# Optimization experiments

Measured on AMD Instinct MI355X. Metric: run time of the kernel, lower is better.

The kernel has to match this reference:

```python
import jax, jax.numpy as jnp
import numpy as np

B, S, H, I, NH, E = 16, 512, 1024, 4096, 16, 8
DH = H // NH
EPS = 1e-12


def layer_norm(x, g, b):
    mu = jnp.mean(x, axis=-1, keepdims=True)
    var = jnp.mean(jnp.square(x - mu), axis=-1, keepdims=True)
    return (x - mu) * jax.lax.rsqrt(var + EPS) * g + b


def setup_inputs() -> dict:
    key = jax.random.key(0)
    ks = jax.random.split(key, 16)
    s_h = 1.0 / np.sqrt(H)
    s_i = 1.0 / np.sqrt(I)
    return {
        "hidden_states": jax.random.normal(ks[0], (B, S, H), jnp.float32),
        "Wq": jax.random.normal(ks[1], (H, H), jnp.float32) * s_h,
        "bq": jnp.zeros((H,), jnp.float32),
        "Wk": jax.random.normal(ks[2], (H, H), jnp.float32) * s_h,
        "bk": jnp.zeros((H,), jnp.float32),
        "Wv": jax.random.normal(ks[3], (H, H), jnp.float32) * s_h,
        "bv": jnp.zeros((H,), jnp.float32),
        "Wo": jax.random.normal(ks[4], (H, H), jnp.float32) * s_h,
        "bo": jnp.zeros((H,), jnp.float32),
        "ln1_g": jnp.ones((H,), jnp.float32),
        "ln1_b": jnp.zeros((H,), jnp.float32),
        "ln2_g": jnp.ones((H,), jnp.float32),
        "ln2_b": jnp.zeros((H,), jnp.float32),
        "gate_W": jax.random.normal(ks[5], (H, E), jnp.float32) * s_h,
        "W_up": jax.random.normal(ks[6], (E, H, I), jnp.float32) * s_h,
        "b_up": jnp.zeros((E, I), jnp.float32),
        "W_down": jax.random.normal(ks[7], (E, I, H), jnp.float32) * s_i,
        "b_down": jnp.zeros((E, H), jnp.float32),
    }


def reference(hidden_states, Wq, bq, Wk, bk, Wv, bv, Wo, bo,
              ln1_g, ln1_b, ln2_g, ln2_b, gate_W, W_up, b_up, W_down, b_down):
    x = hidden_states
    # --- BERT self-attention ---
    q = (x @ Wq + bq).reshape(B, S, NH, DH)
    k = (x @ Wk + bk).reshape(B, S, NH, DH)
    v = (x @ Wv + bv).reshape(B, S, NH, DH)
    scores = jnp.einsum("bqhd,bkhd->bhqk", q, k) / np.sqrt(DH)
    probs = jax.nn.softmax(scores, axis=-1)
    ctx = jnp.einsum("bhqk,bkhd->bqhd", probs, v).reshape(B, S, H)
    # BertSelfOutput: dense + residual + LayerNorm
    attn_out = layer_norm(ctx @ Wo + bo + x, ln1_g, ln1_b)

    # --- feed_forward_chunk: pre-LN, MoE, residual (residual on attn_out) ---
    x_ln = layer_norm(attn_out, ln2_g, ln2_b)
    router_output = jnp.einsum("bsh,he->bse", x_ln, gate_W)
    router_logits = jnp.mean(router_output, axis=1)          # [B, E]
    choice = jnp.argmax(router_logits, axis=-1)              # softmax-argmax == logits-argmax

    # per-sample top-1 expert: gather each sample's expert weights, batched GEMM
    Wu = W_up[choice]                                        # [B, H, I]
    Wd = W_down[choice]                                      # [B, I, H]
    h = jax.nn.gelu(jnp.einsum("bsh,bhi->bsi", x_ln, Wu) + b_up[choice][:, None, :],
                    approximate=False)
    moe = jnp.einsum("bsi,bih->bsh", h, Wd) + b_down[choice][:, None, :]
    layer_output = moe + attn_out
    return (layer_output, router_logits)
```

## Files before the change

kernel.cpp:

```cpp
#include <hip/hip_runtime.h>


typedef __attribute__((ext_vector_type(4))) float f32x4;
typedef __attribute__((ext_vector_type(8))) short s8v;
typedef __attribute__((ext_vector_type(4))) short s4v;
typedef unsigned short u16;

#define DEV static __device__ __forceinline__

DEV u16 f2bf(float f){
  union { float f; unsigned u; } v; v.f = f;
  unsigned r = v.u + 0x7fffu + ((v.u >> 16) & 1u);
  return (u16)(r >> 16);
}

DEV f32x4 mfma16(s8v a, s8v b, f32x4 c){
  return __builtin_amdgcn_mfma_f32_16x16x32_bf16(a, b, c, 0, 0, 0);
}

DEV float wave_sum(float s){
#pragma unroll
  for (int o = 1; o < 64; o <<= 1) s += __shfl_xor(s, o);
  return s;
}

#define ASYNC_COPY16(g, l) \
  __builtin_amdgcn_global_load_lds((const __attribute__((address_space(1))) void*)(g), \
                                   (__attribute__((address_space(3))) void*)(l), 16, 0, 0)

__global__ __launch_bounds__(256) void cvt_bf16(const float* __restrict__ in,
                                                u16* __restrict__ out)
{
  const size_t i = ((size_t)blockIdx.x * 256 + threadIdx.x) * 8;
  f32x4 a = *(const f32x4*)&in[i];
  f32x4 b = *(const f32x4*)&in[i + 4];
  s8v o;
#pragma unroll
  for (int j = 0; j < 4; ++j){ o[j] = (short)f2bf(a[j]); o[4 + j] = (short)f2bf(b[j]); }
  *(s8v*)&out[i] = o;
}

__global__ __launch_bounds__(256) void transpose_w(const float* __restrict__ in,
                                                   u16* __restrict__ out, int R, int C)
{
  __shared__ float t[64][65];
  const size_t bs = (size_t)blockIdx.z * R * (size_t)C;
  in += bs; out += bs;
  const int c0 = blockIdx.x * 64, r0 = blockIdx.y * 64;
  const int tx = threadIdx.x & 63, ty = threadIdx.x >> 6;
#pragma unroll
  for (int j = 0; j < 64; j += 4) t[ty + j][tx] = in[(size_t)(r0 + ty + j) * C + c0 + tx];
  __syncthreads();
#pragma unroll
  for (int j = 0; j < 64; j += 4) out[(size_t)(c0 + ty + j) * R + r0 + tx] = f2bf(t[tx][ty + j]);
}

template<int MODE>
__global__ __launch_bounds__(256, 2) void gemm_bt(
    const u16* __restrict__ A, const u16* __restrict__ Bt,
    const float* __restrict__ bias, void* __restrict__ outp,
    const float* __restrict__ resid, int M, int N, int K,
    const int* __restrict__ choice,
    long aBatch, long outBatch, long residBatch, long btExpert, long biasExpert)
{
  const int z = blockIdx.z;
  if (choice){
    const int e = choice[z];
    Bt   += (size_t)e * btExpert;
    bias += (size_t)e * biasExpert;
  }
  A += (size_t)z * aBatch;

  const int tid = threadIdx.x;
  const int lane = tid & 63, wid = tid >> 6;
  const int hi = lane >> 4, l15 = lane & 15;
  const int wr = wid >> 1, wc = wid & 1;
  const long row0 = (long)blockIdx.x * 128;
  const long col0 = (long)blockIdx.y * 128;

  __shared__ __align__(16) u16 lA[128 * 32];
  __shared__ __align__(16) u16 lB[128 * 32];

  f32x4 acc[4][4];
#pragma unroll
  for (int i = 0; i < 4; ++i)
#pragma unroll
    for (int j = 0; j < 4; ++j) acc[i][j] = f32x4{0.f, 0.f, 0.f, 0.f};

  const int c1 = tid, c2 = tid + 256;
  const u16* sA1 = A  + (row0 + (c1 >> 2)) * (size_t)K + (c1 & 3) * 8;
  const u16* sA2 = A  + (row0 + (c2 >> 2)) * (size_t)K + (c2 & 3) * 8;
  const u16* sB1 = Bt + (col0 + (c1 >> 2)) * (size_t)K + (c1 & 3) * 8;
  const u16* sB2 = Bt + (col0 + (c2 >> 2)) * (size_t)K + (c2 & 3) * 8;
  u16* dA1 = &lA[c1 * 8]; u16* dA2 = &lA[c2 * 8];
  u16* dB1 = &lB[c1 * 8]; u16* dB2 = &lB[c2 * 8];

  for (int kt = 0; kt < K; kt += 32){
    ASYNC_COPY16(sA1, dA1);
    ASYNC_COPY16(sA2, dA2);
    ASYNC_COPY16(sB1, dB1);
    ASYNC_COPY16(sB2, dB2);
    sA1 += 32; sA2 += 32; sB1 += 32; sB2 += 32;
    asm volatile("s_waitcnt vmcnt(0)" ::: "memory");
    __syncthreads();

    s8v af[4], bf[4];
#pragma unroll
    for (int mi = 0; mi < 4; ++mi)
      af[mi] = *(const s8v*)&lA[(wr * 64 + mi * 16 + l15) * 32 + hi * 8];
#pragma unroll
    for (int ni = 0; ni < 4; ++ni)
      bf[ni] = *(const s8v*)&lB[(wc * 64 + ni * 16 + l15) * 32 + hi * 8];
#pragma unroll
    for (int mi = 0; mi < 4; ++mi)
#pragma unroll
      for (int ni = 0; ni < 4; ++ni)
        acc[mi][ni] = mfma16(af[mi], bf[ni], acc[mi][ni]);
    __syncthreads();
  }

#pragma unroll
  for (int mi = 0; mi < 4; ++mi){
    const long rowb = row0 + wr * 64 + mi * 16 + hi * 4;
#pragma unroll
    for (int ni = 0; ni < 4; ++ni){
      const long col = col0 + wc * 64 + ni * 16 + l15;
      const float bv = bias[col];
#pragma unroll
      for (int r = 0; r < 4; ++r){
        const long row = rowb + r;
        float v = acc[mi][ni][r] + bv;
        if (MODE == 2){
          float* o = (float*)outp + (size_t)z * outBatch;
          const float* rs = resid + (size_t)z * residBatch;
          o[row * N + col] = v + rs[row * N + col];
        } else if (MODE == 0){
          u16* o = (u16*)outp + (size_t)z * outBatch;
          o[row * N + col] = f2bf(v);
        } else if (MODE == 1){
          u16* o = (u16*)outp + (size_t)z * outBatch;
          const float gv = 0.5f * v * (1.0f + erff(v * 0.70710678118654752f));
          o[row * N + col] = f2bf(gv);
        } else {
          const int bb = (int)(row >> 9), ss = (int)(row & 511);
          const int hh = (int)(col >> 6), dd = (int)(col & 63);
          ((u16*)outp)[(((size_t)(bb * 16 + hh)) * 64 + dd) * 512 + ss] = f2bf(v);
        }
      }
    }
  }
}

__global__ __launch_bounds__(256) void attn_fwd(
    const u16* __restrict__ qb, const u16* __restrict__ kb,
    const u16* __restrict__ vt, u16* __restrict__ ctx)
{
  const int tid = threadIdx.x;
  const int lane = tid & 63, wid = tid >> 6;
  const int hi = lane >> 4, l15 = lane & 15;
  const int h = blockIdx.y, b = blockIdx.z;
  const int q0 = blockIdx.x * 128 + wid * 32;

  const u16* kp0 = kb + (size_t)b * 512 * 1024 + h * 64;
  const u16* vp0 = vt + ((size_t)(b * 16 + h)) * 64 * 512;

  __shared__ __align__(16) u16 lK[2][64 * 64];
  __shared__ __align__(16) u16 lV[2][64 * 64];
  __shared__ __align__(16) u16 lP[4][2][16][72];

#define STAGE(bsel, k0s) do { \
  _Pragma("unroll") \
  for (int i = 0; i < 2; ++i){ \
    const int idx = i * 256 + tid; \
    const int row = idx >> 3, seg = idx & 7; \
    const int sc = ((seg ^ (row & 7)) << 3); \
    ASYNC_COPY16(kp0 + (size_t)((k0s) + row) * 1024 + sc, &lK[bsel][idx * 8]); \
    ASYNC_COPY16(vp0 + (size_t)row * 512 + (k0s) + sc,    &lV[bsel][idx * 8]); \
  } \
} while (0)

  const u16* qp = qb + ((size_t)b * 512 + q0) * 1024 + h * 64;
  s8v qf[2][2];
#pragma unroll
  for (int qt = 0; qt < 2; ++qt)
#pragma unroll
    for (int st = 0; st < 2; ++st)
      qf[qt][st] = *(const s8v*)&qp[(size_t)(qt * 16 + l15) * 1024 + st * 32 + hi * 8];

  f32x4 o[2][4];
#pragma unroll
  for (int qt = 0; qt < 2; ++qt)
#pragma unroll
    for (int mi = 0; mi < 4; ++mi) o[qt][mi] = f32x4{0.f, 0.f, 0.f, 0.f};
  float mrun[2] = {-3e38f, -3e38f}, lrun[2] = {0.f, 0.f};

  STAGE(0, 0);
  __syncthreads();

  for (int t = 0; t < 8; ++t){
    const int buf = t & 1;
    if (t < 7) STAGE(buf ^ 1, (t + 1) * 64);

    f32x4 s[2][4];
#pragma unroll
    for (int qt = 0; qt < 2; ++qt)
#pragma unroll
      for (int kt = 0; kt < 4; ++kt) s[qt][kt] = f32x4{0.f, 0.f, 0.f, 0.f};
#pragma unroll
    for (int st = 0; st < 2; ++st){
      s8v kf[4];
#pragma unroll
      for (int kt = 0; kt < 4; ++kt){
        const int row = kt * 16 + l15;
        kf[kt] = *(const s8v*)&lK[buf][row * 64 + (((st * 4 + hi) ^ (row & 7)) << 3)];
      }
#pragma unroll
      for (int qt = 0; qt < 2; ++qt)
#pragma unroll
        for (int kt = 0; kt < 4; ++kt)
          s[qt][kt] = mfma16(kf[kt], qf[qt][st], s[qt][kt]);
    }

#pragma unroll
    for (int qt = 0; qt < 2; ++qt){
      float mx = s[qt][0][0];
#pragma unroll
      for (int kt = 0; kt < 4; ++kt)
#pragma unroll
        for (int r = 0; r < 4; ++r) mx = fmaxf(mx, s[qt][kt][r]);
      mx *= 0.125f;
      mx = fmaxf(mx, __shfl_xor(mx, 16));
      mx = fmaxf(mx, __shfl_xor(mx, 32));
      const float mnew = fmaxf(mrun[qt], mx);
      const float alpha = __expf(mrun[qt] - mnew);
      mrun[qt] = mnew;
      float ps = 0.f;
#pragma unroll
      for (int kt = 0; kt < 4; ++kt){
        s4v pk;
#pragma unroll
        for (int r = 0; r < 4; ++r){
          const float p = __expf(s[qt][kt][r] * 0.125f - mnew);
          ps += p; pk[r] = (short)f2bf(p);
        }
        *(s4v*)&lP[wid][qt][l15][kt * 16 + 4 * hi] = pk;
      }
      ps += __shfl_xor(ps, 16);
      ps += __shfl_xor(ps, 32);
      lrun[qt] = lrun[qt] * alpha + ps;
#pragma unroll
      for (int mi = 0; mi < 4; ++mi)
#pragma unroll
        for (int r = 0; r < 4; ++r) o[qt][mi][r] *= alpha;
    }

#pragma unroll
    for (int ks = 0; ks < 2; ++ks){
      s8v vf[4];
#pragma unroll
      for (int mi = 0; mi < 4; ++mi){
        const int row = mi * 16 + l15;
        vf[mi] = *(const s8v*)&lV[buf][row * 64 + (((ks * 4 + hi) ^ (row & 7)) << 3)];
      }
#pragma unroll
      for (int qt = 0; qt < 2; ++qt){
        const s8v pf = *(const s8v*)&lP[wid][qt][l15][ks * 32 + 8 * hi];
#pragma unroll
        for (int mi = 0; mi < 4; ++mi)
          o[qt][mi] = mfma16(vf[mi], pf, o[qt][mi]);
      }
    }
    __syncthreads();
  }
#undef STAGE

#pragma unroll
  for (int qt = 0; qt < 2; ++qt){
    const float inv = 1.f / lrun[qt];
    u16* cp = ctx + ((size_t)b * 512 + q0 + qt * 16 + l15) * 1024 + h * 64;
#pragma unroll
    for (int mi = 0; mi < 4; ++mi)
#pragma unroll
      for (int r = 0; r < 4; ++r)
        cp[mi * 16 + 4 * hi + r] = f2bf(o[qt][mi][r] * inv);
  }
}

__global__ __launch_bounds__(256, 2) void ln_inplace(float* __restrict__ x,
    const float* __restrict__ g, const float* __restrict__ be)
{
  const int row = blockIdx.x * 4 + (threadIdx.x >> 6);
  const int lane = threadIdx.x & 63;
  float* p = x + (size_t)row * 1024;
  f32x4 v[4];
#pragma unroll
  for (int c = 0; c < 4; ++c) v[c] = *(const f32x4*)&p[c * 256 + lane * 4];
  float s = 0.f;
#pragma unroll
  for (int c = 0; c < 4; ++c){ s += v[c][0] + v[c][1] + v[c][2] + v[c][3]; }
  const float mu = wave_sum(s) * (1.f / 1024.f);
  float s2 = 0.f;
#pragma unroll
  for (int c = 0; c < 4; ++c)
#pragma unroll
    for (int j = 0; j < 4; ++j){ const float d = v[c][j] - mu; s2 += d * d; }
  const float rs = rsqrtf(wave_sum(s2) * (1.f / 1024.f) + 1e-12f);
#pragma unroll
  for (int c = 0; c < 4; ++c){
    const f32x4 gg = *(const f32x4*)&g[c * 256 + lane * 4];
    const f32x4 bb = *(const f32x4*)&be[c * 256 + lane * 4];
    f32x4 ov;
#pragma unroll
    for (int j = 0; j < 4; ++j) ov[j] = (v[c][j] - mu) * rs * gg[j] + bb[j];
    *(f32x4*)&p[c * 256 + lane * 4] = ov;
  }
}

__global__ __launch_bounds__(256, 2) void ln2_colsum(
    const float* __restrict__ attn, const float* __restrict__ g, const float* __restrict__ be,
    u16* __restrict__ xln, float* __restrict__ colsum)
{
  const int b = blockIdx.y;
  const int wid = threadIdx.x >> 6, lane = threadIdx.x & 63;
  __shared__ float cacc[1024];
  for (int i = threadIdx.x; i < 1024; i += 256) cacc[i] = 0.f;
  __syncthreads();
  float acc[16];
#pragma unroll
  for (int i = 0; i < 16; ++i) acc[i] = 0.f;
  const int rbase = b * 512 + blockIdx.x * 64 + wid * 16;
  for (int rr = 0; rr < 16; ++rr){
    const float* p = attn + (size_t)(rbase + rr) * 1024;
    f32x4 v[4];
#pragma unroll
    for (int c = 0; c < 4; ++c) v[c] = *(const f32x4*)&p[c * 256 + lane * 4];
    float s = 0.f;
#pragma unroll
    for (int c = 0; c < 4; ++c) s += v[c][0] + v[c][1] + v[c][2] + v[c][3];
    const float mu = wave_sum(s) * (1.f / 1024.f);
    float s2 = 0.f;
#pragma unroll
    for (int c = 0; c < 4; ++c)
#pragma unroll
      for (int j = 0; j < 4; ++j){ const float d = v[c][j] - mu; s2 += d * d; }
    const float rs = rsqrtf(wave_sum(s2) * (1.f / 1024.f) + 1e-12f);
    u16* op = xln + (size_t)(rbase + rr) * 1024;
#pragma unroll
    for (int c = 0; c < 4; ++c){
      const f32x4 gg = *(const f32x4*)&g[c * 256 + lane * 4];
      const f32x4 bb = *(const f32x4*)&be[c * 256 + lane * 4];
      s4v ov;
#pragma unroll
      for (int j = 0; j < 4; ++j){
        const float y = (v[c][j] - mu) * rs * gg[j] + bb[j];
        acc[c * 4 + j] += y;
        ov[j] = (short)f2bf(y);
      }
      *(s4v*)&op[c * 256 + lane * 4] = ov;
    }
  }
#pragma unroll
  for (int c = 0; c < 4; ++c)
#pragma unroll
    for (int j = 0; j < 4; ++j)
      atomicAdd(&cacc[c * 256 + lane * 4 + j], acc[c * 4 + j]);
  __syncthreads();
  for (int i = threadIdx.x; i < 1024; i += 256) atomicAdd(&colsum[b * 1024 + i], cacc[i]);
}

__global__ void router_argmax(const float* __restrict__ colsum, const float* __restrict__ gate,
                              float* __restrict__ logits, int* __restrict__ choice)
{
  const int b = blockIdx.x, lane = threadIdx.x;
  float pa[8];
#pragma unroll
  for (int e = 0; e < 8; ++e) pa[e] = 0.f;
  for (int it = 0; it < 16; ++it){
    const int hh = it * 64 + lane;
    const float c = colsum[b * 1024 + hh];
    const float* gp = gate + (size_t)hh * 8;
#pragma unroll
    for (int e = 0; e < 8; ++e) pa[e] += c * gp[e];
  }
#pragma unroll
  for (int e = 0; e < 8; ++e) pa[e] = wave_sum(pa[e]);
  if (lane == 0){
    float best = -3e38f; int bi = 0;
#pragma unroll
    for (int e = 0; e < 8; ++e){
      const float lg = pa[e] * (1.f / 512.f);
      logits[b * 8 + e] = lg;
      if (lg > best){ best = lg; bi = e; }
    }
    choice[b] = bi;
  }
}

extern "C" void kernel_launch(void* const* d_in, const int* in_sizes, int n_in,
                              void* d_out, int out_size, void* d_ws, size_t ws_size,
                              hipStream_t stream)
{
  const float* x    = (const float*)d_in[0];
  const float* Wq   = (const float*)d_in[1];
  const float* bq   = (const float*)d_in[2];
  const float* Wk   = (const float*)d_in[3];
  const float* bk   = (const float*)d_in[4];
  const float* Wv   = (const float*)d_in[5];
  const float* bv   = (const float*)d_in[6];
  const float* Wo   = (const float*)d_in[7];
  const float* bo   = (const float*)d_in[8];
  const float* ln1g = (const float*)d_in[9];
  const float* ln1b = (const float*)d_in[10];
  const float* ln2g = (const float*)d_in[11];
  const float* ln2b = (const float*)d_in[12];
  const float* gate = (const float*)d_in[13];
  const float* Wup  = (const float*)d_in[14];
  const float* bup  = (const float*)d_in[15];
  const float* Wdn  = (const float*)d_in[16];
  const float* bdn  = (const float*)d_in[17];

  size_t off = 0;
  char* wsb = (char*)d_ws;
  auto take = [&](size_t n) -> void* {
    void* p = wsb + off; off += (n + 255) & ~(size_t)255; return p;
  };
  u16*   x_bf  = (u16*)take(8192ull * 1024 * 2);
  u16*   Wqt   = (u16*)take(1024ull * 1024 * 2);
  u16*   Wkt   = (u16*)take(1024ull * 1024 * 2);
  u16*   Wvt   = (u16*)take(1024ull * 1024 * 2);
  u16*   Wot   = (u16*)take(1024ull * 1024 * 2);
  u16*   q_bf  = (u16*)take(8192ull * 1024 * 2);
  u16*   k_bf  = (u16*)take(8192ull * 1024 * 2);
  u16*   vt_bf = (u16*)take(8192ull * 1024 * 2);
  float* tmp   = (float*)take(8192ull * 1024 * 4);
  u16*   Wupt  = (u16*)take(8ull * 4096 * 1024 * 2);
  u16*   Wdnt  = (u16*)take(8ull * 1024 * 4096 * 2);
  u16*   h_bf  = (u16*)take(8192ull * 4096 * 2);
  float* colsum = (float*)take(16ull * 1024 * 4);
  int*   choice = (int*)take(256);

  u16* ctx = x_bf;
  u16* xln = q_bf;
  float* logits = (float*)d_out + 8388608;

  cvt_bf16<<<4096, 256, 0, stream>>>(x, x_bf);
  transpose_w<<<dim3(16, 16, 1), 256, 0, stream>>>(Wq,  Wqt,  1024, 1024);
  transpose_w<<<dim3(16, 16, 1), 256, 0, stream>>>(Wk,  Wkt,  1024, 1024);
  transpose_w<<<dim3(16, 16, 1), 256, 0, stream>>>(Wv,  Wvt,  1024, 1024);
  transpose_w<<<dim3(16, 16, 1), 256, 0, stream>>>(Wo,  Wot,  1024, 1024);
  transpose_w<<<dim3(64, 16, 8), 256, 0, stream>>>(Wup, Wupt, 1024, 4096);
  transpose_w<<<dim3(16, 64, 8), 256, 0, stream>>>(Wdn, Wdnt, 4096, 1024);

  gemm_bt<0><<<dim3(64, 8, 1), 256, 0, stream>>>(x_bf, Wqt, bq, q_bf,  nullptr,
      8192, 1024, 1024, nullptr, 0, 0, 0, 0, 0);
  gemm_bt<0><<<dim3(64, 8, 1), 256, 0, stream>>>(x_bf, Wkt, bk, k_bf,  nullptr,
      8192, 1024, 1024, nullptr, 0, 0, 0, 0, 0);
  gemm_bt<3><<<dim3(64, 8, 1), 256, 0, stream>>>(x_bf, Wvt, bv, vt_bf, nullptr,
      8192, 1024, 1024, nullptr, 0, 0, 0, 0, 0);

  attn_fwd<<<dim3(4, 16, 16), 256, 0, stream>>>(q_bf, k_bf, vt_bf, ctx);

  gemm_bt<2><<<dim3(64, 8, 1), 256, 0, stream>>>(ctx, Wot, bo, tmp, x,
      8192, 1024, 1024, nullptr, 0, 0, 0, 0, 0);
  ln_inplace<<<2048, 256, 0, stream>>>(tmp, ln1g, ln1b);

  hipMemsetAsync(colsum, 0, 16 * 1024 * sizeof(float), stream);
  ln2_colsum<<<dim3(8, 16), 256, 0, stream>>>(tmp, ln2g, ln2b, xln, colsum);
  router_argmax<<<16, 64, 0, stream>>>(colsum, gate, logits, choice);

  gemm_bt<1><<<dim3(4, 32, 16), 256, 0, stream>>>(xln, Wupt, bup, h_bf, nullptr,
      512, 4096, 1024, choice, 512ll * 1024, 512ll * 4096, 0, 4096ll * 1024, 4096);
  gemm_bt<2><<<dim3(4, 8, 16), 256, 0, stream>>>(h_bf, Wdnt, bdn, d_out, tmp,
      512, 1024, 4096, choice, 512ll * 4096, 512ll * 1024, 512ll * 1024, 1024ll * 4096, 1024);
}
```

Measured before the change: 552.7 us.

## Fuse QKV GEMM, merge both LayerNorms, double-buffer GEMM LDS, swizzle MoE blocks

The three Q/K/V projections become one N=3072 GEMM, relying on the transposed weights sitting contiguously in the workspace and on a concatenated bias. A new epilogue mode routes each column segment to q, k or the transposed v layout. LN1 and LN2 are merged into one pass that writes attn_out and the bf16 LN2 output and accumulates the router column sums, which removes a separate full-tensor read and write. The GEMM mainloop now uses two LDS buffers so the next K tile's async copy is issued before the current tile's MFMAs, and the MoE GEMMs remap block IDs across XCDs for better L2 locality. The loads are no longer followed by an explicit vmcnt wait, so correctness depends on the barrier waiting for the async copies, and the larger LDS footprint may reduce occupancy.

```diff
diff --git a/kernel.cpp b/kernel.cpp
--- a/kernel.cpp
+++ b/kernel.cpp
@@ -55,15 +55,26 @@
   for (int j = 0; j < 64; j += 4) out[(size_t)(c0 + ty + j) * R + r0 + tx] = f2bf(t[tx][ty + j]);
 }
 
-template<int MODE>
+template<int MODE, bool SWZ>
 __global__ __launch_bounds__(256, 2) void gemm_bt(
     const u16* __restrict__ A, const u16* __restrict__ Bt,
     const float* __restrict__ bias, void* __restrict__ outp,
     const float* __restrict__ resid, int M, int N, int K,
     const int* __restrict__ choice,
-    long aBatch, long outBatch, long residBatch, long btExpert, long biasExpert)
-{
-  const int z = blockIdx.z;
+    long aBatch, long outBatch, long residBatch, long btExpert, long biasExpert,
+    void* __restrict__ out2, void* __restrict__ out3)
+{
+  int bx, by, bz;
+  if (SWZ){
+    const int nx = gridDim.x, ny = gridDim.y;
+    const int nwg = nx * ny * gridDim.z;
+    int id = blockIdx.x + nx * (blockIdx.y + ny * blockIdx.z);
+    if ((nwg & 7) == 0){ const int q = nwg >> 3; id = (id & 7) * q + (id >> 3); }
+    bx = id % nx; const int r2 = id / nx; by = r2 % ny; bz = r2 / ny;
+  } else {
+    bx = blockIdx.x; by = blockIdx.y; bz = blockIdx.z;
+  }
+  const int z = bz;
   if (choice){
     const int e = choice[z];
     Bt   += (size_t)e * btExpert;
@@ -75,11 +86,11 @@
   const int lane = tid & 63, wid = tid >> 6;
   const int hi = lane >> 4, l15 = lane & 15;
   const int wr = wid >> 1, wc = wid & 1;
-  const long row0 = (long)blockIdx.x * 128;
-  const long col0 = (long)blockIdx.y * 128;
-
-  __shared__ __align__(16) u16 lA[128 * 32];
-  __shared__ __align__(16) u16 lB[128 * 32];
+  const long row0 = (long)bx * 128;
+  const long col0 = (long)by * 128;
+
+  __shared__ __align__(16) u16 lA[2][128 * 32];
+  __shared__ __align__(16) u16 lB[2][128 * 32];
 
   f32x4 acc[4][4];
 #pragma unroll
@@ -92,32 +103,37 @@
   const u16* sA2 = A  + (row0 + (c2 >> 2)) * (size_t)K + (c2 & 3) * 8;
   const u16* sB1 = Bt + (col0 + (c1 >> 2)) * (size_t)K + (c1 & 3) * 8;
   const u16* sB2 = Bt + (col0 + (c2 >> 2)) * (size_t)K + (c2 & 3) * 8;
-  u16* dA1 = &lA[c1 * 8]; u16* dA2 = &lA[c2 * 8];
-  u16* dB1 = &lB[c1 * 8]; u16* dB2 = &lB[c2 * 8];
-
-  for (int kt = 0; kt < K; kt += 32){
-    ASYNC_COPY16(sA1, dA1);
-    ASYNC_COPY16(sA2, dA2);
-    ASYNC_COPY16(sB1, dB1);
-    ASYNC_COPY16(sB2, dB2);
-    sA1 += 32; sA2 += 32; sB1 += 32; sB2 += 32;
-    asm volatile("s_waitcnt vmcnt(0)" ::: "memory");
+
+#define GSTAGE(bsel) do { \
+  ASYNC_COPY16(sA1, &lA[bsel][c1 * 8]); \
+  ASYNC_COPY16(sA2, &lA[bsel][c2 * 8]); \
+  ASYNC_COPY16(sB1, &lB[bsel][c1 * 8]); \
+  ASYNC_COPY16(sB2, &lB[bsel][c2 * 8]); \
+  sA1 += 32; sA2 += 32; sB1 += 32; sB2 += 32; \
+} while (0)
+
+  const int nk = K >> 5;
+  GSTAGE(0);
+  __syncthreads();
+
+  for (int t = 0; t < nk; ++t){
+    const int cur = t & 1;
+    if (t + 1 < nk) GSTAGE(cur ^ 1);
+    s8v af[4], bfr[4];
+#pragma unroll
+    for (int mi = 0; mi < 4; ++mi)
+      af[mi] = *(const s8v*)&lA[cur][(wr * 64 + mi * 16 + l15) * 32 + hi * 8];
+#pragma unroll
+    for (int ni = 0; ni < 4; ++ni)
+      bfr[ni] = *(const s8v*)&lB[cur][(wc * 64 + ni * 16 + l15) * 32 + hi * 8];
+#pragma unroll
+    for (int mi = 0; mi < 4; ++mi)
+#pragma unroll
+      for (int ni = 0; ni < 4; ++ni)
+        acc[mi][ni] = mfma16(af[mi], bfr[ni], acc[mi][ni]);
     __syncthreads();
-
-    s8v af[4], bf[4];
-#pragma unroll
-    for (int mi = 0; mi < 4; ++mi)
-      af[mi] = *(const s8v*)&lA[(wr * 64 + mi * 16 + l15) * 32 + hi * 8];
-#pragma unroll
-    for (int ni = 0; ni < 4; ++ni)
-      bf[ni] = *(const s8v*)&lB[(wc * 64 + ni * 16 + l15) * 32 + hi * 8];
-#pragma unroll
-    for (int mi = 0; mi < 4; ++mi)
-#pragma unroll
-      for (int ni = 0; ni < 4; ++ni)
-        acc[mi][ni] = mfma16(af[mi], bf[ni], acc[mi][ni]);
-    __syncthreads();
-  }
+  }
+#undef GSTAGE
 
 #pragma unroll
   for (int mi = 0; mi < 4; ++mi){
@@ -141,10 +157,20 @@
           u16* o = (u16*)outp + (size_t)z * outBatch;
           const float gv = 0.5f * v * (1.0f + erff(v * 0.70710678118654752f));
           o[row * N + col] = f2bf(gv);
-        } else {
+        } else if (MODE == 3){
           const int bb = (int)(row >> 9), ss = (int)(row & 511);
           const int hh = (int)(col >> 6), dd = (int)(col & 63);
           ((u16*)outp)[(((size_t)(bb * 16 + hh)) * 64 + dd) * 512 + ss] = f2bf(v);
+        } else {
+          const int seg = (int)(col >> 10), lc = (int)(col & 1023);
+          const u16 bv16 = f2bf(v);
+          if (seg == 0)      ((u16*)outp)[row * 1024 + lc] = bv16;
+          else if (seg == 1) ((u16*)out2)[row * 1024 + lc] = bv16;
+          else {
+            const int bb = (int)(row >> 9), ss = (int)(row & 511);
+            const int hh = lc >> 6, dd = lc & 63;
+            ((u16*)out3)[(((size_t)(bb * 16 + hh)) * 64 + dd) * 512 + ss] = bv16;
+          }
         }
       }
     }
@@ -286,38 +312,9 @@
   }
 }
 
-__global__ __launch_bounds__(256, 2) void ln_inplace(float* __restrict__ x,
-    const float* __restrict__ g, const float* __restrict__ be)
-{
-  const int row = blockIdx.x * 4 + (threadIdx.x >> 6);
-  const int lane = threadIdx.x & 63;
-  float* p = x + (size_t)row * 1024;
-  f32x4 v[4];
-#pragma unroll
-  for (int c = 0; c < 4; ++c) v[c] = *(const f32x4*)&p[c * 256 + lane * 4];
-  float s = 0.f;
-#pragma unroll
-  for (int c = 0; c < 4; ++c){ s += v[c][0] + v[c][1] + v[c][2] + v[c][3]; }
-  const float mu = wave_sum(s) * (1.f / 1024.f);
-  float s2 = 0.f;
-#pragma unroll
-  for (int c = 0; c < 4; ++c)
-#pragma unroll
-    for (int j = 0; j < 4; ++j){ const float d = v[c][j] - mu; s2 += d * d; }
-  const float rs = rsqrtf(wave_sum(s2) * (1.f / 1024.f) + 1e-12f);
-#pragma unroll
-  for (int c = 0; c < 4; ++c){
-    const f32x4 gg = *(const f32x4*)&g[c * 256 + lane * 4];
-    const f32x4 bb = *(const f32x4*)&be[c * 256 + lane * 4];
-    f32x4 ov;
-#pragma unroll
-    for (int j = 0; j < 4; ++j) ov[j] = (v[c][j] - mu) * rs * gg[j] + bb[j];
-    *(f32x4*)&p[c * 256 + lane * 4] = ov;
-  }
-}
-
-__global__ __launch_bounds__(256, 2) void ln2_colsum(
-    const float* __restrict__ attn, const float* __restrict__ g, const float* __restrict__ be,
+__global__ __launch_bounds__(256, 2) void ln12_colsum(
+    float* __restrict__ t, const float* __restrict__ g1, const float* __restrict__ b1,
+    const float* __restrict__ g2, const float* __restrict__ b2,
     u16* __restrict__ xln, float* __restrict__ colsum)
 {
   const int b = blockIdx.y;
@@ -330,7 +327,7 @@
   for (int i = 0; i < 16; ++i) acc[i] = 0.f;
   const int rbase = b * 512 + blockIdx.x * 64 + wid * 16;
   for (int rr = 0; rr < 16; ++rr){
-    const float* p = attn + (size_t)(rbase + rr) * 1024;
+    float* p = t + (size_t)(rbase + rr) * 1024;
     f32x4 v[4];
 #pragma unroll
     for (int c = 0; c < 4; ++c) v[c] = *(const f32x4*)&p[c * 256 + lane * 4];
@@ -344,15 +341,34 @@
 #pragma unroll
       for (int j = 0; j < 4; ++j){ const float d = v[c][j] - mu; s2 += d * d; }
     const float rs = rsqrtf(wave_sum(s2) * (1.f / 1024.f) + 1e-12f);
+    float y1s = 0.f;
+#pragma unroll
+    for (int c = 0; c < 4; ++c){
+      const f32x4 gg = *(const f32x4*)&g1[c * 256 + lane * 4];
+      const f32x4 bb = *(const f32x4*)&b1[c * 256 + lane * 4];
+#pragma unroll
+      for (int j = 0; j < 4; ++j){
+        v[c][j] = (v[c][j] - mu) * rs * gg[j] + bb[j];
+        y1s += v[c][j];
+      }
+      *(f32x4*)&p[c * 256 + lane * 4] = v[c];
+    }
+    const float mu2 = wave_sum(y1s) * (1.f / 1024.f);
+    float s22 = 0.f;
+#pragma unroll
+    for (int c = 0; c < 4; ++c)
+#pragma unroll
+      for (int j = 0; j < 4; ++j){ const float d = v[c][j] - mu2; s22 += d * d; }
+    const float rs2 = rsqrtf(wave_sum(s22) * (1.f / 1024.f) + 1e-12f);
     u16* op = xln + (size_t)(rbase + rr) * 1024;
 #pragma unroll
     for (int c = 0; c < 4; ++c){
-      const f32x4 gg = *(const f32x4*)&g[c * 256 + lane * 4];
-      const f32x4 bb = *(const f32x4*)&be[c * 256 + lane * 4];
+      const f32x4 gg = *(const f32x4*)&g2[c * 256 + lane * 4];
+      const f32x4 bb = *(const f32x4*)&b2[c * 256 + lane * 4];
       s4v ov;
 #pragma unroll
       for (int j = 0; j < 4; ++j){
-        const float y = (v[c][j] - mu) * rs * gg[j] + bb[j];
+        const float y = (v[c][j] - mu2) * rs2 * gg[j] + bb[j];
         acc[c * 4 + j] += y;
         ov[j] = (short)f2bf(y);
       }
@@ -438,6 +454,7 @@
   u16*   h_bf  = (u16*)take(8192ull * 4096 * 2);
   float* colsum = (float*)take(16ull * 1024 * 4);
   int*   choice = (int*)take(256);
+  float* qkvb  = (float*)take(3072 * 4);
 
   u16* ctx = x_bf;
   u16* xln = q_bf;
@@ -450,26 +467,25 @@
   transpose_w<<<dim3(16, 16, 1), 256, 0, stream>>>(Wo,  Wot,  1024, 1024);
   transpose_w<<<dim3(64, 16, 8), 256, 0, stream>>>(Wup, Wupt, 1024, 4096);
   transpose_w<<<dim3(16, 64, 8), 256, 0, stream>>>(Wdn, Wdnt, 4096, 1024);
-
-  gemm_bt<0><<<dim3(64, 8, 1), 256, 0, stream>>>(x_bf, Wqt, bq, q_bf,  nullptr,
-      8192, 1024, 1024, nullptr, 0, 0, 0, 0, 0);
-  gemm_bt<0><<<dim3(64, 8, 1), 256, 0, stream>>>(x_bf, Wkt, bk, k_bf,  nullptr,
-      8192, 1024, 1024, nullptr, 0, 0, 0, 0, 0);
-  gemm_bt<3><<<dim3(64, 8, 1), 256, 0, stream>>>(x_bf, Wvt, bv, vt_bf, nullptr,
-      8192, 1024, 1024, nullptr, 0, 0, 0, 0, 0);
+  hipMemcpyAsync(qkvb,        bq, 1024 * 4, hipMemcpyDeviceToDevice, stream);
+  hipMemcpyAsync(qkvb + 1024, bk, 1024 * 4, hipMemcpyDeviceToDevice, stream);
+  hipMemcpyAsync(qkvb + 2048, bv, 1024 * 4, hipMemcpyDeviceToDevice, stream);
+
+  gemm_bt<4, false><<<dim3(64, 24, 1), 256, 0, stream>>>(x_bf, Wqt, qkvb, q_bf,
+      nullptr, 8192, 3072, 1024, nullptr, 0, 0, 0, 0, 0, k_bf, vt_bf);
 
   attn_fwd<<<dim3(4, 16, 16), 256, 0, stream>>>(q_bf, k_bf, vt_bf, ctx);
 
-  gemm_bt<2><<<dim3(64, 8, 1), 256, 0, stream>>>(ctx, Wot, bo, tmp, x,
-      8192, 1024, 1024, nullptr, 0, 0, 0, 0, 0);
-  ln_inplace<<<2048, 256, 0, stream>>>(tmp, ln1g, ln1b);
-
+  gemm_bt<2, false><<<dim3(64, 8, 1), 256, 0, stream>>>(ctx, Wot, bo, tmp, x,
+      8192, 1024, 1024, nullptr, 0, 0, 0, 0, 0, nullptr, nullptr);
   hipMemsetAsync(colsum, 0, 16 * 1024 * sizeof(float), stream);
-  ln2_colsum<<<dim3(8, 16), 256, 0, stream>>>(tmp, ln2g, ln2b, xln, colsum);
+  ln12_colsum<<<dim3(8, 16), 256, 0, stream>>>(tmp, ln1g, ln1b, ln2g, ln2b, xln, colsum);
   router_argmax<<<16, 64, 0, stream>>>(colsum, gate, logits, choice);
 
-  gemm_bt<1><<<dim3(4, 32, 16), 256, 0, stream>>>(xln, Wupt, bup, h_bf, nullptr,
-      512, 4096, 1024, choice, 512ll * 1024, 512ll * 4096, 0, 4096ll * 1024, 4096);
-  gemm_bt<2><<<dim3(4, 8, 16), 256, 0, stream>>>(h_bf, Wdnt, bdn, d_out, tmp,
-      512, 1024, 4096, choice, 512ll * 4096, 512ll * 1024, 512ll * 1024, 1024ll * 4096, 1024);
-}
+  gemm_bt<1, true><<<dim3(4, 32, 16), 256, 0, stream>>>(xln, Wupt, bup, h_bf, nullptr,
+      512, 4096, 1024, choice, 512ll * 1024, 512ll * 4096, 0, 4096ll * 1024, 4096,
+      nullptr, nullptr);
+  gemm_bt<2, true><<<dim3(4, 8, 16), 256, 0, stream>>>(h_bf, Wdnt, bdn, d_out, tmp,
+      512, 1024, 4096, choice, 512ll * 4096, 512ll * 1024, 512ll * 1024, 1024ll * 4096, 1024,
+      nullptr, nullptr);
+}
```

Measured after the change: 535.0 us. 3.2% less time.
